# Optimization experiments

Measured on AMD Instinct MI355X. Metric: run time of the kernel, lower is better.

The kernel has to match this reference:

```python
import jax, jax.numpy as jnp
import numpy as np
from jax import lax

D_MODEL = 768
BATCH = 16
SEQ = 2048
N_BLOCKS = D_MODEL // 3
LN_EPS = 1e-5


def setup_inputs() -> dict:
    key = jax.random.key(0)
    ks = jax.random.split(key, 4)
    scale = 1.0 / np.sqrt(D_MODEL)
    x = jax.random.normal(ks[0], (BATCH, SEQ, D_MODEL), dtype=jnp.float32)
    W_biv = jax.random.normal(ks[1], (D_MODEL, D_MODEL), dtype=jnp.float32) * scale
    b_biv = jnp.zeros((D_MODEL,), dtype=jnp.float32)
    W_decay = jax.random.normal(ks[2], (1, D_MODEL), dtype=jnp.float32) * scale
    b_decay = jnp.full((1,), 1.4, dtype=jnp.float32)  # nn.init.constant_(decay_proj.bias, 1.4)
    W_in = jax.random.normal(ks[3], (D_MODEL, D_MODEL), dtype=jnp.float32) * scale
    b_in = jnp.zeros((D_MODEL,), dtype=jnp.float32)
    ln_gamma = jnp.ones((D_MODEL,), dtype=jnp.float32)
    ln_beta = jnp.zeros((D_MODEL,), dtype=jnp.float32)
    return {"x": x, "W_biv": W_biv, "b_biv": b_biv, "W_decay": W_decay,
            "b_decay": b_decay, "W_in": W_in, "b_in": b_in,
            "ln_gamma": ln_gamma, "ln_beta": ln_beta}


def _quat_rotate_blocks(h_blocks, biv):
    """h_blocks, biv: (batch, n_blocks, 3) -> rotated (batch, n_blocks, 3)."""
    norm_b = jnp.maximum(jnp.linalg.norm(biv, axis=-1, keepdims=True), 1e-8)
    half = norm_b * 0.5
    w = jnp.cos(half)[..., 0]
    s = (jnp.sin(half) / norm_b)[..., 0]
    # note the original maps bivector components in reversed order
    qx = s * biv[..., 2]
    qy = -s * biv[..., 1]
    qz = s * biv[..., 0]
    vx, vy, vz = h_blocks[..., 0], h_blocks[..., 1], h_blocks[..., 2]
    tx = 2.0 * (qy * vz - qz * vy)
    ty = 2.0 * (qz * vx - qx * vz)
    tz = 2.0 * (qx * vy - qy * vx)
    rx = vx + w * tx + (qy * tz - qz * ty)
    ry = vy + w * ty + (qz * tx - qx * tz)
    rz = vz + w * tz + (qx * ty - qy * tx)
    return jnp.stack([rx, ry, rz], axis=-1)


def reference(x, W_biv, b_biv, W_decay, b_decay, W_in, b_in, ln_gamma, ln_beta):
    B, S, D = x.shape
    nb = D // 3
    # precompute all per-timestep projections as big GEMMs
    biv = (jnp.einsum('bsd,ed->bse', x, W_biv) + b_biv).reshape(B, S, nb, 3)
    decay = jax.nn.sigmoid(jnp.einsum('bsd,ed->bse', x, W_decay) + b_decay)  # (B,S,1)
    inj = jnp.einsum('bsd,ed->bse', x, W_in) + b_in  # (B,S,D)

    def step(h, t):
        biv_t, decay_t, inj_t = t
        rot = _quat_rotate_blocks(h.reshape(B, nb, 3), biv_t).reshape(B, D)
        h_next = decay_t * rot + inj_t
        return h_next, h_next

    xs = (jnp.moveaxis(biv, 1, 0), jnp.moveaxis(decay, 1, 0), jnp.moveaxis(inj, 1, 0))
    h0 = jnp.zeros((B, D), dtype=x.dtype)
    _, out = lax.scan(step, h0, xs)  # (S,B,D)
    out = jnp.moveaxis(out, 0, 1)  # (B,S,D)

    mean = jnp.mean(out, axis=-1, keepdims=True)
    var = jnp.mean(jnp.square(out - mean), axis=-1, keepdims=True)
    normed = (out - mean) * lax.rsqrt(var + LN_EPS) * ln_gamma + ln_beta
    return normed + x
```

## Files before the change

### kernel.cpp

```cpp
#include <hip/hip_runtime.h>
#include <stdint.h>

#define D_MODEL 768
#define BATCH   16
#define SEQ     2048
#define M_ROWS  (BATCH * SEQ)
#define LN_EPS  1e-5f

#define CHUNKS  64
#define CLEN    (SEQ / CHUNKS)
#define PFB     8

typedef __attribute__((ext_vector_type(4))) float        f32x4;
typedef __attribute__((ext_vector_type(8))) __bf16       bf16x8;
typedef __attribute__((ext_vector_type(2))) unsigned int u32x2;

__device__ __forceinline__ unsigned short f2bf(float f) {
    union { float f; uint32_t u; } v; v.f = f;
    uint32_t u = v.u;
    uint32_t r = (u + 0x7FFFu + ((u >> 16) & 1u)) >> 16;
    return (unsigned short)r;
}
__device__ __forceinline__ float bf2f(unsigned short u) {
    union { uint32_t u; float f; } v; v.u = (uint32_t)u << 16; return v.f;
}
__device__ __forceinline__ float bfx(u32x2 v, int k) {
    unsigned int w = (k & 2) ? v[1] : v[0];
    return bf2f((unsigned short)(w >> ((k & 1) * 16)));
}

__device__ __forceinline__ void gload_lds16(const void* g, void* l) {
    __builtin_amdgcn_global_load_lds(
        (const __attribute__((address_space(1))) unsigned int*)g,
        (__attribute__((address_space(3))) unsigned int*)l,
        16, 0, 0);
}

__global__ __launch_bounds__(256) void k_conv_decay(
    const float* __restrict__ x, const float* __restrict__ Wd,
    const float* __restrict__ bd, unsigned short* __restrict__ xb,
    float* __restrict__ decay)
{
    int row = blockIdx.x;
    int i   = threadIdx.x;
    const float* xr = x + (size_t)row * D_MODEL;
    float v0 = xr[i], v1 = xr[i + 256], v2 = xr[i + 512];
    unsigned short* xbr = xb + (size_t)row * D_MODEL;
    xbr[i] = f2bf(v0); xbr[i + 256] = f2bf(v1); xbr[i + 512] = f2bf(v2);

    float part = v0 * Wd[i] + v1 * Wd[i + 256] + v2 * Wd[i + 512];
    #pragma unroll
    for (int off = 32; off; off >>= 1) part += __shfl_down(part, off);
    __shared__ float wsum[4];
    int wid = i >> 6, lane = i & 63;
    if (lane == 0) wsum[wid] = part;
    __syncthreads();
    if (i == 0) {
        float s = wsum[0] + wsum[1] + wsum[2] + wsum[3] + bd[0];
        decay[row] = 1.f / (1.f + __expf(-s));
    }
}

__global__ __launch_bounds__(256) void k_conv_w(
    const float* __restrict__ Wb, const float* __restrict__ Wi,
    unsigned short* __restrict__ Wdst)
{
    const int NW = D_MODEL * D_MODEL;
    int g = blockIdx.x * 256 + threadIdx.x;
    int base = g * 4;
    unsigned short* dst = Wdst + base;
    const float* src;
    if (base < NW) { src = Wb + base; }
    else           { src = Wi + (base - NW); }
    float4 v = *(const float4*)src;
    ushort4 o;
    o.x = f2bf(v.x); o.y = f2bf(v.y); o.z = f2bf(v.z); o.w = f2bf(v.w);
    *(ushort4*)dst = o;
}

#define GBM 256
#define GBN 256
#define GNBX 6
#define GNBY 128
#define NT   12

__global__ __launch_bounds__(512, 2) void k_gemm_fused(
    const unsigned short* __restrict__ A,
    const unsigned short* __restrict__ Bw,
    const float* __restrict__ bias_biv, const float* __restrict__ bias_in,
    u32x2* __restrict__ bivq, u32x2* __restrict__ injq)
{
    extern __shared__ unsigned short LDSBUF[];
    unsigned short* LA = LDSBUF;
    unsigned short* LB = LDSBUF + 32768;

    int id  = blockIdx.x;
    int swz = (id & 7) * 96 + (id >> 3);
    int bxc = swz % GNBX, byr = swz / GNBX;
    int m0 = byr * GBM, n0 = bxc * GBN;

    int tid  = threadIdx.x;
    int wid  = tid >> 6, lane = tid & 63;
    int wm = wid >> 2, wn = wid & 3;
    int rl = lane & 15, kq = lane >> 4;
    int sl = kq ^ ((rl >> 1) & 3);
    int aoff = (wm * 128 + rl) * 32 + sl * 8;
    int boff = (wn * 64  + rl) * 32 + sl * 8;

    f32x4 acc[8][4] = {};

    #define STAGE_HALF(DBUF, KT, HH) do {                                        \
        _Pragma("unroll")                                                        \
        for (int p = 0; p < 2; ++p) {                                            \
            int idx = p * 512 + tid;                                             \
            int row = idx >> 2;                                                  \
            int ss  = ((idx & 3) ^ ((idx >> 3) & 3)) * 8;  \
            gload_lds16(A  + (size_t)(m0 + row) * D_MODEL + (KT) * 64 + (HH) * 32 + ss, \
                        LA + (DBUF) * 16384 + (HH) * 8192 + idx * 8);            \
            gload_lds16(Bw + (size_t)(n0 + row) * D_MODEL + (KT) * 64 + (HH) * 32 + ss, \
                        LB + (DBUF) * 16384 + (HH) * 8192 + idx * 8);            \
        }                                                                        \
    } while (0)

    #define PHASE(D, H, DOSTAGE, SBUF, SKT, SHH, WAITSTR) do {                   \
        bf16x8 af[8], bfv[4];                                                    \
        const unsigned short* pa = LA + (D) * 16384 + (H) * 8192 + aoff;         \
        const unsigned short* pb = LB + (D) * 16384 + (H) * 8192 + boff;         \
        _Pragma("unroll")                                                        \
        for (int i = 0; i < 8; ++i) af[i]  = *(const bf16x8*)(pa + i * 512);     \
        _Pragma("unroll")                                                        \
        for (int j = 0; j < 4; ++j) bfv[j] = *(const bf16x8*)(pb + j * 512);     \
        if (DOSTAGE) STAGE_HALF(SBUF, SKT, SHH);                                 \
        asm volatile(WAITSTR ::: "memory");                                      \
        asm volatile("s_barrier" ::: "memory");                                  \
        asm volatile("s_waitcnt lgkmcnt(0)" ::: "memory");                       \
        __builtin_amdgcn_sched_barrier(0);                                       \
        __builtin_amdgcn_s_setprio(1);                                           \
        _Pragma("unroll")                                                        \
        for (int i = 0; i < 8; ++i)                                              \
            _Pragma("unroll")                                                    \
            for (int j = 0; j < 4; ++j)                                          \
                acc[i][j] = __builtin_amdgcn_mfma_f32_16x16x32_bf16(             \
                    af[i], bfv[j], acc[i][j], 0, 0, 0);                          \
        __builtin_amdgcn_s_setprio(0);                                           \
        asm volatile("s_barrier" ::: "memory");                                  \
    } while (0)

    STAGE_HALF(0, 0, 0);
    STAGE_HALF(0, 0, 1);
    STAGE_HALF(1, 1, 0);
    asm volatile("s_waitcnt vmcnt(8)" ::: "memory");
    asm volatile("s_barrier" ::: "memory");

    for (int t = 0; t < 10; ++t) {
        int cur = t & 1;
        PHASE(cur, 0, true, cur ^ 1, t + 1, 1, "s_waitcnt vmcnt(8)");
        PHASE(cur, 1, true, cur,     t + 2, 0, "s_waitcnt vmcnt(8)");
    }
    PHASE(0, 0, true,  1, 11, 1, "s_waitcnt vmcnt(8)");
    PHASE(0, 1, false, 0, 0,  0, "s_waitcnt vmcnt(4)");
    PHASE(1, 0, false, 0, 0,  0, "s_waitcnt vmcnt(0)");
    PHASE(1, 1, false, 0, 0,  0, "");

    #undef PHASE
    #undef STAGE_HALF

    u32x2* Cq; const float* bias; int nloc;
    if (n0 < D_MODEL) { Cq = bivq; bias = bias_biv; nloc = n0; }
    else              { Cq = injq; bias = bias_in;  nloc = n0 - D_MODEL; }
    int cl = lane & 15;
    int qbase = (m0 >> 2) + wm * 32 + (lane >> 4);
    #pragma unroll
    for (int j = 0; j < 4; ++j) {
        int col = nloc + wn * 64 + j * 16 + cl;
        float bs = bias[col];
        #pragma unroll
        for (int i = 0; i < 8; ++i) {
            f32x4 a = acc[i][j];
            unsigned int lo = (unsigned int)f2bf(a[0] + bs) | ((unsigned int)f2bf(a[1] + bs) << 16);
            unsigned int hi = (unsigned int)f2bf(a[2] + bs) | ((unsigned int)f2bf(a[3] + bs) << 16);
            u32x2 pk = {lo, hi};
            Cq[(size_t)(qbase + i * 4) * D_MODEL + col] = pk;
        }
    }
}

#define QSTEP_CORE(BX,BY,BZ, IX,IY,IZ, DD)                              \
    {   float n2   = (BX)*(BX) + (BY)*(BY) + (BZ)*(BZ);                 \
        float nrm  = fmaxf(__builtin_sqrtf(n2), 1e-8f);                 \
        float half = 0.5f * nrm;                                        \
        float w = __cosf(half);                                         \
        float s = __sinf(half) / nrm;                                   \
        float qx = s * (BZ), qy = -s * (BY), qz = s * (BX);             \
        float tx = 2.f * (qy * hz - qz * hy);                           \
        float ty = 2.f * (qz * hx - qx * hz);                           \
        float tz = 2.f * (qx * hy - qy * hx);                           \
        float rx = hx + w * tx + (qy * tz - qz * ty);                   \
        float ry = hy + w * ty + (qz * tx - qx * tz);                   \
        float rz = hz + w * tz + (qx * ty - qy * tx);                   \
        hx = fmaf((DD), rx, (IX));                                      \
        hy = fmaf((DD), ry, (IY));                                      \
        hz = fmaf((DD), rz, (IZ));                                      \
        float nQw = w * Qw - qx * Qx - qy * Qy - qz * Qz;               \
        float nQx = w * Qx + Qw * qx + (qy * Qz - qz * Qy);             \
        float nQy = w * Qy + Qw * qy + (qz * Qx - qx * Qz);             \
        float nQz = w * Qz + Qw * qz + (qx * Qy - qy * Qx);             \
        Qw = nQw; Qx = nQx; Qy = nQy; Qz = nQz;                         \
        S *= (DD);                                                      \
    }

__global__ __launch_bounds__(256) void k_scan_p1(
    const u32x2* __restrict__ bivq, const u32x2* __restrict__ injq,
    const float* __restrict__ decay,
    float* __restrict__ ops)
{
    int j = threadIdx.x;
    int c = blockIdx.x & (CHUNKS - 1);
    int b = blockIdx.x >> 6;
    size_t qrow = ((size_t)b * SEQ + (size_t)c * CLEN) >> 2;
    const u32x2* bv = bivq + qrow * D_MODEL + 3 * j;
    const u32x2* ij = injq + qrow * D_MODEL + 3 * j;
    const float* dk = decay + (size_t)b * SEQ + c * CLEN;

    u32x2 Ab0, Ab1, Ab2, Ai0, Ai1, Ai2; f32x4 Ad;
    u32x2 Bb0, Bb1, Bb2, Bi0, Bi1, Bi2; f32x4 Bd;

    #define LOADQ1(P, q)                                                  \
        P##b0 = bv[(size_t)(q) * D_MODEL + 0];                            \
        P##b1 = bv[(size_t)(q) * D_MODEL + 1];                            \
        P##b2 = bv[(size_t)(q) * D_MODEL + 2];                            \
        P##i0 = ij[(size_t)(q) * D_MODEL + 0];                            \
        P##i1 = ij[(size_t)(q) * D_MODEL + 1];                            \
        P##i2 = ij[(size_t)(q) * D_MODEL + 2];                            \
        P##d  = *(const f32x4*)(dk + (q) * 4);

    #define PROC41(P)                                                     \
        _Pragma("unroll")                                                 \
        for (int k = 0; k < 4; ++k) {                                     \
            float bx = bfx(P##b0, k), by = bfx(P##b1, k), bz = bfx(P##b2, k); \
            float ix = bfx(P##i0, k), iy = bfx(P##i1, k), iz = bfx(P##i2, k); \
            float d = P##d[k];                                            \
            QSTEP_CORE(bx, by, bz, ix, iy, iz, d)                         \
        }

    float hx = 0.f, hy = 0.f, hz = 0.f;
    float Qw = 1.f, Qx = 0.f, Qy = 0.f, Qz = 0.f, S = 1.f;

    LOADQ1(A, 0)
    LOADQ1(B, 1)
    #pragma unroll
    for (int q0 = 0; q0 < CLEN / 4; q0 += 2) {
        PROC41(A)
        if (q0 + 2 < CLEN / 4) { LOADQ1(A, q0 + 2) }
        PROC41(B)
        if (q0 + 3 < CLEN / 4) { LOADQ1(B, q0 + 3) }
    }
    #undef LOADQ1
    #undef PROC41

    float* op = ops + ((size_t)(b * CHUNKS + c) * 256 + j) * 8;
    f32x4 o0 = {Qw, Qx, Qy, Qz};
    f32x4 o1 = {S, hx, hy, hz};
    *(f32x4*)op = o0;
    *(f32x4*)(op + 4) = o1;
}

__global__ __launch_bounds__(64) void k_scan_p2(
    const float* __restrict__ ops, float* __restrict__ hs)
{
    int gid = blockIdx.x * 64 + threadIdx.x;
    int j = gid & 255, b = gid >> 8;

    float q0[PFB], q1[PFB], q2[PFB], q3[PFB], sc[PFB], o0[PFB], o1[PFB], o2[PFB];
    #pragma unroll
    for (int p = 0; p < PFB; ++p) {
        const float* op = ops + ((size_t)(b * CHUNKS + p) * 256 + j) * 8;
        f32x4 a = *(const f32x4*)op, bb = *(const f32x4*)(op + 4);
        q0[p] = a[0]; q1[p] = a[1]; q2[p] = a[2]; q3[p] = a[3];
        sc[p] = bb[0]; o0[p] = bb[1]; o1[p] = bb[2]; o2[p] = bb[3];
    }
    float hx = 0.f, hy = 0.f, hz = 0.f;
    for (int c0 = 0; c0 < CHUNKS; c0 += PFB) {
        #pragma unroll
        for (int p = 0; p < PFB; ++p) {
            int c = c0 + p;
            float* h = hs + ((size_t)(b * CHUNKS + c) * 256 + j) * 3;
            h[0] = hx; h[1] = hy; h[2] = hz;
            float w = q0[p], qx = q1[p], qy = q2[p], qz = q3[p];
            float s = sc[p], bx = o0[p], by = o1[p], bz = o2[p];
            int cn = c + PFB;
            if (cn < CHUNKS) {
                const float* op = ops + ((size_t)(b * CHUNKS + cn) * 256 + j) * 8;
                f32x4 a = *(const f32x4*)op, bb = *(const f32x4*)(op + 4);
                q0[p] = a[0]; q1[p] = a[1]; q2[p] = a[2]; q3[p] = a[3];
                sc[p] = bb[0]; o0[p] = bb[1]; o1[p] = bb[2]; o2[p] = bb[3];
            }
            float tx = 2.f * (qy * hz - qz * hy);
            float ty = 2.f * (qz * hx - qx * hz);
            float tz = 2.f * (qx * hy - qy * hx);
            float rx = hx + w * tx + (qy * tz - qz * ty);
            float ry = hy + w * ty + (qz * tx - qx * tz);
            float rz = hz + w * tz + (qx * ty - qy * tx);
            hx = fmaf(s, rx, bx);
            hy = fmaf(s, ry, by);
            hz = fmaf(s, rz, bz);
        }
    }
}

__global__ __launch_bounds__(256) void k_scan_p3(
    const u32x2* __restrict__ bivq, const u32x2* __restrict__ injq,
    const float* __restrict__ decay, const float* __restrict__ hs,
    const float* __restrict__ x, const float* __restrict__ gamma,
    const float* __restrict__ beta, float* __restrict__ out)
{
    int blk = blockIdx.x;
    int c = blk & (CHUNKS - 1);
    int b = blk >> 6;
    int j = threadIdx.x;
    size_t rowbase = ((size_t)b * SEQ + (size_t)c * CLEN) * D_MODEL + (size_t)j * 3;
    size_t qrow    = ((size_t)b * SEQ + (size_t)c * CLEN) >> 2;
    const u32x2* bv = bivq + qrow * D_MODEL + 3 * j;
    const u32x2* ij = injq + qrow * D_MODEL + 3 * j;
    const float* xr = x   + rowbase;
    float*       po = out + rowbase;
    const float* dk = decay + (size_t)b * SEQ + c * CLEN;
    const float* h0 = hs + ((size_t)(b * CHUNKS + c) * 256 + j) * 3;
    float hx = h0[0], hy = h0[1], hz = h0[2];
    float Qw = 1.f, Qx = 0.f, Qy = 0.f, Qz = 0.f, S = 1.f;

    float g0 = gamma[j * 3], g1 = gamma[j * 3 + 1], g2 = gamma[j * 3 + 2];
    float e0 = beta[j * 3],  e1 = beta[j * 3 + 1],  e2 = beta[j * 3 + 2];

    __shared__ float sb[8];
    __shared__ float mv[2];
    int wid = j >> 6, lane = j & 63;

    u32x2 Ab0, Ab1, Ab2, Ai0, Ai1, Ai2; f32x4 Ad;
    float Ax0, Ax1, Ax2, Ax3, Ax4, Ax5, Ax6, Ax7, Ax8, Ax9, Ax10, Ax11;
    u32x2 Bb0, Bb1, Bb2, Bi0, Bi1, Bi2; f32x4 Bd;
    float Bx0, Bx1, Bx2, Bx3, Bx4, Bx5, Bx6, Bx7, Bx8, Bx9, Bx10, Bx11;

    #define LOADQ3(P, q)                                                  \
        P##b0 = bv[(size_t)(q) * D_MODEL + 0];                            \
        P##b1 = bv[(size_t)(q) * D_MODEL + 1];                            \
        P##b2 = bv[(size_t)(q) * D_MODEL + 2];                            \
        P##i0 = ij[(size_t)(q) * D_MODEL + 0];                            \
        P##i1 = ij[(size_t)(q) * D_MODEL + 1];                            \
        P##i2 = ij[(size_t)(q) * D_MODEL + 2];                            \
        P##d  = *(const f32x4*)(dk + (q) * 4);                            \
        P##x0  = xr[((size_t)(q) * 4 + 0) * D_MODEL + 0];                 \
        P##x1  = xr[((size_t)(q) * 4 + 0) * D_MODEL + 1];                 \
        P##x2  = xr[((size_t)(q) * 4 + 0) * D_MODEL + 2];                 \
        P##x3  = xr[((size_t)(q) * 4 + 1) * D_MODEL + 0];                 \
        P##x4  = xr[((size_t)(q) * 4 + 1) * D_MODEL + 1];                 \
        P##x5  = xr[((size_t)(q) * 4 + 1) * D_MODEL + 2];                 \
        P##x6  = xr[((size_t)(q) * 4 + 2) * D_MODEL + 0];                 \
        P##x7  = xr[((size_t)(q) * 4 + 2) * D_MODEL + 1];                 \
        P##x8  = xr[((size_t)(q) * 4 + 2) * D_MODEL + 2];                 \
        P##x9  = xr[((size_t)(q) * 4 + 3) * D_MODEL + 0];                 \
        P##x10 = xr[((size_t)(q) * 4 + 3) * D_MODEL + 1];                 \
        P##x11 = xr[((size_t)(q) * 4 + 3) * D_MODEL + 2];

    #define PROC43(P, QBASE)                                              \
    {   { float xa = P##x0,  xbv = P##x1,  xc = P##x2;                    \
          STEP3X(P, 0, (QBASE) * 4 + 0, xa, xbv, xc) }                    \
        { float xa = P##x3,  xbv = P##x4,  xc = P##x5;                    \
          STEP3X(P, 1, (QBASE) * 4 + 1, xa, xbv, xc) }                    \
        { float xa = P##x6,  xbv = P##x7,  xc = P##x8;                    \
          STEP3X(P, 2, (QBASE) * 4 + 2, xa, xbv, xc) }                    \
        { float xa = P##x9,  xbv = P##x10, xc = P##x11;                   \
          STEP3X(P, 3, (QBASE) * 4 + 3, xa, xbv, xc) }                    \
    }

    #define STEP3X(P, k, T, XA, XB, XC)                                   \
    {   float bx = bfx(P##b0, k), by = bfx(P##b1, k), bz = bfx(P##b2, k); \
        float ix = bfx(P##i0, k), iy = bfx(P##i1, k), iz = bfx(P##i2, k); \
        float d = P##d[k];                                                \
        QSTEP_CORE(bx, by, bz, ix, iy, iz, d)                             \
        float sp = hx + hy + hz;                                          \
        float qp = hx * hx + hy * hy + hz * hz;                           \
        _Pragma("unroll")                                                 \
        for (int off = 32; off; off >>= 1) {                              \
            sp += __shfl_down(sp, off);                                   \
            qp += __shfl_down(qp, off);                                   \
        }                                                                 \
        if (lane == 0) { sb[wid] = sp; sb[wid + 4] = qp; }                \
        __syncthreads();                                                  \
        if (j == 0) {                                                     \
            float Ssum = sb[0] + sb[1] + sb[2] + sb[3];                   \
            float Qsum = sb[4] + sb[5] + sb[6] + sb[7];                   \
            float mean = Ssum * (1.f / 768.f);                            \
            float var  = Qsum * (1.f / 768.f) - mean * mean;              \
            mv[0] = mean; mv[1] = rsqrtf(var + LN_EPS);                   \
        }                                                                 \
        __syncthreads();                                                  \
        float mean = mv[0], rstd = mv[1];                                 \
        float* o2 = po + (size_t)(T) * D_MODEL;                           \
        o2[0] = (hx - mean) * rstd * g0 + e0 + (XA);                      \
        o2[1] = (hy - mean) * rstd * g1 + e1 + (XB);                      \
        o2[2] = (hz - mean) * rstd * g2 + e2 + (XC);                      \
    }

    LOADQ3(A, 0)
    LOADQ3(B, 1)
    #pragma unroll
    for (int q0 = 0; q0 < CLEN / 4; q0 += 2) {
        PROC43(A, q0)
        if (q0 + 2 < CLEN / 4) { LOADQ3(A, q0 + 2) }
        PROC43(B, q0 + 1)
        if (q0 + 3 < CLEN / 4) { LOADQ3(B, q0 + 3) }
    }
    (void)Qw; (void)Qx; (void)Qy; (void)Qz; (void)S;
}

extern "C" void kernel_launch(void* const* d_in, const int* in_sizes, int n_in,
                              void* d_out, int out_size, void* d_ws, size_t ws_size,
                              hipStream_t stream) {
    const float* x     = (const float*)d_in[0];
    const float* W_biv = (const float*)d_in[1];
    const float* b_biv = (const float*)d_in[2];
    const float* W_dec = (const float*)d_in[3];
    const float* b_dec = (const float*)d_in[4];
    const float* W_in  = (const float*)d_in[5];
    const float* b_in  = (const float*)d_in[6];
    const float* gamma = (const float*)d_in[7];
    const float* beta  = (const float*)d_in[8];
    float* out = (float*)d_out;

    char* ws = (char*)d_ws;
    unsigned short* xb    = (unsigned short*)(ws);
    unsigned short* Wcat  = (unsigned short*)(ws + 50331648);
    float*          decay = (float*)         (ws + 52690944);
    u32x2*          bivq  = (u32x2*)         (ws + 52822016);
    u32x2*          injq  = (u32x2*)         (ws + 103153664);
    float*          ops   = (float*)(ws);
    float*          hs    = (float*)(ws + 8388608);

    (void)in_sizes; (void)n_in; (void)out_size; (void)ws_size;

    hipFuncSetAttribute((const void*)k_gemm_fused,
                        hipFuncAttributeMaxDynamicSharedMemorySize, 131072);

    k_conv_decay<<<M_ROWS, 256, 0, stream>>>(x, W_dec, b_dec, xb, decay);
    k_conv_w    <<<1152,   256, 0, stream>>>(W_biv, W_in, Wcat);
    k_gemm_fused<<<GNBX * GNBY, 512, 131072, stream>>>(xb, Wcat, b_biv, b_in, bivq, injq);
    k_scan_p1   <<<1024, 256, 0, stream>>>(bivq, injq, decay, ops);
    k_scan_p2   <<<64,   64,  0, stream>>>(ops, hs);
    k_scan_p3   <<<1024, 256, 0, stream>>>(bivq, injq, decay, hs, x, gamma, beta, out);
}
```

Before: 220.1 us.

## Defer scan LayerNorm to a per-row wave pass over shared-memory hidden states

The phase-3 scan no longer runs a block-wide LayerNorm reduction with two __syncthreads at every timestep. Each thread now advances its recurrence over the whole chunk and stores the hidden states to shared memory packed as bf16. After a single barrier, each wave normalises whole rows using shuffle-xor reductions and float4 loads of x and stores of the output. This removes per-step block barriers from the serial recurrence and vectorises the epilogue. The cost is 48 KB of LDS per block, which may limit occupancy, and extra rounding from storing hidden states as bf16 before normalisation.

```diff
diff --git a/kernel.cpp b/kernel.cpp
--- a/kernel.cpp
+++ b/kernel.cpp
@@ -207,6 +207,24 @@
         float nQz = w * Qz + Qw * qz + (qx * Qy - qy * Qx);             \
         Qw = nQw; Qx = nQx; Qy = nQy; Qz = nQz;                         \
         S *= (DD);                                                      \
+    }
+
+#define QSTEP_H(BX,BY,BZ, IX,IY,IZ, DD)                                 \
+    {   float n2   = (BX)*(BX) + (BY)*(BY) + (BZ)*(BZ);                 \
+        float nrm  = fmaxf(__builtin_sqrtf(n2), 1e-8f);                 \
+        float half = 0.5f * nrm;                                        \
+        float w = __cosf(half);                                         \
+        float s = __sinf(half) / nrm;                                   \
+        float qx = s * (BZ), qy = -s * (BY), qz = s * (BX);             \
+        float tx = 2.f * (qy * hz - qz * hy);                           \
+        float ty = 2.f * (qz * hx - qx * hz);                           \
+        float tz = 2.f * (qx * hy - qy * hx);                           \
+        float rx = hx + w * tx + (qy * tz - qz * ty);                   \
+        float ry = hy + w * ty + (qz * tx - qx * tz);                   \
+        float rz = hz + w * tz + (qx * ty - qy * tx);                   \
+        hx = fmaf((DD), rx, (IX));                                      \
+        hy = fmaf((DD), ry, (IY));                                      \
+        hz = fmaf((DD), rz, (IZ));                                      \
     }
 
 __global__ __launch_bounds__(256) void k_scan_p1(
@@ -318,100 +336,105 @@
     int c = blk & (CHUNKS - 1);
     int b = blk >> 6;
     int j = threadIdx.x;
-    size_t rowbase = ((size_t)b * SEQ + (size_t)c * CLEN) * D_MODEL + (size_t)j * 3;
-    size_t qrow    = ((size_t)b * SEQ + (size_t)c * CLEN) >> 2;
+    size_t row0 = (size_t)b * SEQ + (size_t)c * CLEN;
+    size_t qrow = row0 >> 2;
     const u32x2* bv = bivq + qrow * D_MODEL + 3 * j;
     const u32x2* ij = injq + qrow * D_MODEL + 3 * j;
-    const float* xr = x   + rowbase;
-    float*       po = out + rowbase;
-    const float* dk = decay + (size_t)b * SEQ + c * CLEN;
+    const float* dk = decay + row0;
     const float* h0 = hs + ((size_t)(b * CHUNKS + c) * 256 + j) * 3;
     float hx = h0[0], hy = h0[1], hz = h0[2];
-    float Qw = 1.f, Qx = 0.f, Qy = 0.f, Qz = 0.f, S = 1.f;
-
-    float g0 = gamma[j * 3], g1 = gamma[j * 3 + 1], g2 = gamma[j * 3 + 2];
-    float e0 = beta[j * 3],  e1 = beta[j * 3 + 1],  e2 = beta[j * 3 + 2];
-
-    __shared__ float sb[8];
-    __shared__ float mv[2];
-    int wid = j >> 6, lane = j & 63;
+
+    __shared__ uint32_t       hxyS[CLEN * 256];
+    __shared__ unsigned short hzS [CLEN * 256];
 
     u32x2 Ab0, Ab1, Ab2, Ai0, Ai1, Ai2; f32x4 Ad;
-    float Ax0, Ax1, Ax2, Ax3, Ax4, Ax5, Ax6, Ax7, Ax8, Ax9, Ax10, Ax11;
     u32x2 Bb0, Bb1, Bb2, Bi0, Bi1, Bi2; f32x4 Bd;
-    float Bx0, Bx1, Bx2, Bx3, Bx4, Bx5, Bx6, Bx7, Bx8, Bx9, Bx10, Bx11;
-
-    #define LOADQ3(P, q)                                                  \
+
+    #define LOADQH(P, q)                                                  \
         P##b0 = bv[(size_t)(q) * D_MODEL + 0];                            \
         P##b1 = bv[(size_t)(q) * D_MODEL + 1];                            \
         P##b2 = bv[(size_t)(q) * D_MODEL + 2];                            \
         P##i0 = ij[(size_t)(q) * D_MODEL + 0];                            \
         P##i1 = ij[(size_t)(q) * D_MODEL + 1];                            \
         P##i2 = ij[(size_t)(q) * D_MODEL + 2];                            \
-        P##d  = *(const f32x4*)(dk + (q) * 4);                            \
-        P##x0  = xr[((size_t)(q) * 4 + 0) * D_MODEL + 0];                 \
-        P##x1  = xr[((size_t)(q) * 4 + 0) * D_MODEL + 1];                 \
-        P##x2  = xr[((size_t)(q) * 4 + 0) * D_MODEL + 2];                 \
-        P##x3  = xr[((size_t)(q) * 4 + 1) * D_MODEL + 0];                 \
-        P##x4  = xr[((size_t)(q) * 4 + 1) * D_MODEL + 1];                 \
-        P##x5  = xr[((size_t)(q) * 4 + 1) * D_MODEL + 2];                 \
-        P##x6  = xr[((size_t)(q) * 4 + 2) * D_MODEL + 0];                 \
-        P##x7  = xr[((size_t)(q) * 4 + 2) * D_MODEL + 1];                 \
-        P##x8  = xr[((size_t)(q) * 4 + 2) * D_MODEL + 2];                 \
-        P##x9  = xr[((size_t)(q) * 4 + 3) * D_MODEL + 0];                 \
-        P##x10 = xr[((size_t)(q) * 4 + 3) * D_MODEL + 1];                 \
-        P##x11 = xr[((size_t)(q) * 4 + 3) * D_MODEL + 2];
-
-    #define PROC43(P, QBASE)                                              \
-    {   { float xa = P##x0,  xbv = P##x1,  xc = P##x2;                    \
-          STEP3X(P, 0, (QBASE) * 4 + 0, xa, xbv, xc) }                    \
-        { float xa = P##x3,  xbv = P##x4,  xc = P##x5;                    \
-          STEP3X(P, 1, (QBASE) * 4 + 1, xa, xbv, xc) }                    \
-        { float xa = P##x6,  xbv = P##x7,  xc = P##x8;                    \
-          STEP3X(P, 2, (QBASE) * 4 + 2, xa, xbv, xc) }                    \
-        { float xa = P##x9,  xbv = P##x10, xc = P##x11;                   \
-          STEP3X(P, 3, (QBASE) * 4 + 3, xa, xbv, xc) }                    \
-    }
-
-    #define STEP3X(P, k, T, XA, XB, XC)                                   \
-    {   float bx = bfx(P##b0, k), by = bfx(P##b1, k), bz = bfx(P##b2, k); \
-        float ix = bfx(P##i0, k), iy = bfx(P##i1, k), iz = bfx(P##i2, k); \
-        float d = P##d[k];                                                \
-        QSTEP_CORE(bx, by, bz, ix, iy, iz, d)                             \
-        float sp = hx + hy + hz;                                          \
-        float qp = hx * hx + hy * hy + hz * hz;                           \
+        P##d  = *(const f32x4*)(dk + (q) * 4);
+
+    #define PROC4H(P, QBASE)                                              \
         _Pragma("unroll")                                                 \
-        for (int off = 32; off; off >>= 1) {                              \
-            sp += __shfl_down(sp, off);                                   \
-            qp += __shfl_down(qp, off);                                   \
-        }                                                                 \
-        if (lane == 0) { sb[wid] = sp; sb[wid + 4] = qp; }                \
-        __syncthreads();                                                  \
-        if (j == 0) {                                                     \
-            float Ssum = sb[0] + sb[1] + sb[2] + sb[3];                   \
-            float Qsum = sb[4] + sb[5] + sb[6] + sb[7];                   \
-            float mean = Ssum * (1.f / 768.f);                            \
-            float var  = Qsum * (1.f / 768.f) - mean * mean;              \
-            mv[0] = mean; mv[1] = rsqrtf(var + LN_EPS);                   \
-        }                                                                 \
-        __syncthreads();                                                  \
-        float mean = mv[0], rstd = mv[1];                                 \
-        float* o2 = po + (size_t)(T) * D_MODEL;                           \
-        o2[0] = (hx - mean) * rstd * g0 + e0 + (XA);                      \
-        o2[1] = (hy - mean) * rstd * g1 + e1 + (XB);                      \
-        o2[2] = (hz - mean) * rstd * g2 + e2 + (XC);                      \
-    }
-
-    LOADQ3(A, 0)
-    LOADQ3(B, 1)
+        for (int k = 0; k < 4; ++k) {                                     \
+            float bx = bfx(P##b0, k), by = bfx(P##b1, k), bz = bfx(P##b2, k); \
+            float ix = bfx(P##i0, k), iy = bfx(P##i1, k), iz = bfx(P##i2, k); \
+            float d = P##d[k];                                            \
+            QSTEP_H(bx, by, bz, ix, iy, iz, d)                            \
+            int tt = (QBASE) * 4 + k;                                     \
+            hxyS[tt * 256 + j] = (uint32_t)f2bf(hx) | ((uint32_t)f2bf(hy) << 16); \
+            hzS [tt * 256 + j] = f2bf(hz);                                \
+        }
+
+    LOADQH(A, 0)
+    LOADQH(B, 1)
     #pragma unroll
     for (int q0 = 0; q0 < CLEN / 4; q0 += 2) {
-        PROC43(A, q0)
-        if (q0 + 2 < CLEN / 4) { LOADQ3(A, q0 + 2) }
-        PROC43(B, q0 + 1)
-        if (q0 + 3 < CLEN / 4) { LOADQ3(B, q0 + 3) }
-    }
-    (void)Qw; (void)Qx; (void)Qy; (void)Qz; (void)S;
+        PROC4H(A, q0)
+        if (q0 + 2 < CLEN / 4) { LOADQH(A, q0 + 2) }
+        PROC4H(B, q0 + 1)
+        if (q0 + 3 < CLEN / 4) { LOADQH(B, q0 + 3) }
+    }
+    #undef LOADQH
+    #undef PROC4H
+
+    __syncthreads();
+
+    int wid = j >> 6, lane = j & 63;
+    const float4* g4 = (const float4*)(gamma + lane * 12);
+    const float4* e4 = (const float4*)(beta  + lane * 12);
+    float4 G0 = g4[0], G1 = g4[1], G2 = g4[2];
+    float4 E0 = e4[0], E1 = e4[1], E2 = e4[2];
+    const float* xbase = x   + row0 * D_MODEL;
+    float*       obase = out + row0 * D_MODEL;
+
+    for (int r = wid; r < CLEN; r += 4) {
+        uint4   hv = *(const uint4*)  &hxyS[r * 256 + 4 * lane];
+        ushort4 zv = *(const ushort4*)&hzS [r * 256 + 4 * lane];
+        float h[12];
+        h[0]  = bf2f((unsigned short)(hv.x & 0xFFFF)); h[1]  = bf2f((unsigned short)(hv.x >> 16)); h[2]  = bf2f(zv.x);
+        h[3]  = bf2f((unsigned short)(hv.y & 0xFFFF)); h[4]  = bf2f((unsigned short)(hv.y >> 16)); h[5]  = bf2f(zv.y);
+        h[6]  = bf2f((unsigned short)(hv.z & 0xFFFF)); h[7]  = bf2f((unsigned short)(hv.z >> 16)); h[8]  = bf2f(zv.z);
+        h[9]  = bf2f((unsigned short)(hv.w & 0xFFFF)); h[10] = bf2f((unsigned short)(hv.w >> 16)); h[11] = bf2f(zv.w);
+        float sp = 0.f, qp = 0.f;
+        #pragma unroll
+        for (int k = 0; k < 12; ++k) { sp += h[k]; qp += h[k] * h[k]; }
+        #pragma unroll
+        for (int off = 1; off < 64; off <<= 1) {
+            sp += __shfl_xor(sp, off);
+            qp += __shfl_xor(qp, off);
+        }
+        float mean = sp * (1.f / 768.f);
+        float var  = qp * (1.f / 768.f) - mean * mean;
+        float rstd = rsqrtf(var + LN_EPS);
+
+        const float* xr2 = xbase + (size_t)r * D_MODEL + lane * 12;
+        float*       or2 = obase + (size_t)r * D_MODEL + lane * 12;
+        float4 X0 = *(const float4*)(xr2 + 0);
+        float4 X1 = *(const float4*)(xr2 + 4);
+        float4 X2 = *(const float4*)(xr2 + 8);
+        float4 O0, O1, O2;
+        O0.x = (h[0]  - mean) * rstd * G0.x + E0.x + X0.x;
+        O0.y = (h[1]  - mean) * rstd * G0.y + E0.y + X0.y;
+        O0.z = (h[2]  - mean) * rstd * G0.z + E0.z + X0.z;
+        O0.w = (h[3]  - mean) * rstd * G0.w + E0.w + X0.w;
+        O1.x = (h[4]  - mean) * rstd * G1.x + E1.x + X1.x;
+        O1.y = (h[5]  - mean) * rstd * G1.y + E1.y + X1.y;
+        O1.z = (h[6]  - mean) * rstd * G1.z + E1.z + X1.z;
+        O1.w = (h[7]  - mean) * rstd * G1.w + E1.w + X1.w;
+        O2.x = (h[8]  - mean) * rstd * G2.x + E2.x + X2.x;
+        O2.y = (h[9]  - mean) * rstd * G2.y + E2.y + X2.y;
+        O2.z = (h[10] - mean) * rstd * G2.z + E2.z + X2.z;
+        O2.w = (h[11] - mean) * rstd * G2.w + E2.w + X2.w;
+        *(float4*)(or2 + 0) = O0;
+        *(float4*)(or2 + 4) = O1;
+        *(float4*)(or2 + 8) = O2;
+    }
 }
 
 extern "C" void kernel_launch(void* const* d_in, const int* in_sizes, int n_in,
```

Result: no change. 221.3 us (+0.5%).
